# Optimization experiments

Measured on AMD Instinct MI355X. Metric: run time of the kernel, lower is better.

The kernel has to match this reference:

```python
import jax, jax.numpy as jnp
import numpy as np

B, L, E, MODES = 32, 2048, 512, 32  # batch, seq_len, d_model, kept Fourier modes (mode_select='low')


def setup_inputs() -> dict:
    key = jax.random.key(0)
    ks = jax.random.split(key, 6)
    scale = 1.0 / (E * E)  # FourierBlock scale = 1/(in_channels*out_channels), torch.rand init
    lin = E ** -0.5
    return {
        "queries": jax.random.normal(ks[0], (B, L, E), jnp.float32),
        "Wq": jax.random.normal(ks[1], (E, E), jnp.float32) * lin,
        "bq": jnp.zeros((E,), jnp.float32),
        "W1r": jax.random.uniform(ks[2], (E, E, MODES), jnp.float32) * scale,
        "W1i": jax.random.uniform(ks[3], (E, E, MODES), jnp.float32) * scale,
        "Wo": jax.random.normal(ks[4], (E, E), jnp.float32) * lin,
        "bo": jnp.zeros((E,), jnp.float32),
    }


def reference(queries, Wq, bq, W1r, W1i, Wo, bo):
    Bn, Ln, En = queries.shape
    # query projection
    q = queries @ Wq.T + bq                                    # (B, L, E)
    # FourierBlock: FFT along time, keep low `MODES` bins, complex channel mixing, inverse FFT
    xf = jnp.fft.rfft(q, axis=1)                               # (B, L//2+1, E) complex64
    W1 = (W1r + 1j * W1i).astype(jnp.complex64)                # (E_in, E_out, M)
    sel = xf[:, :MODES, :]                                     # (B, M, E) selected modes (mode_select='low')
    out_sel = jnp.einsum('bmi,iom->bmo', sel, W1)              # per-mode complex E x E mixing
    nfreq = Ln // 2 + 1
    out_ft = jnp.zeros((Bn, nfreq, En), jnp.complex64).at[:, :MODES, :].set(out_sel)
    x = jnp.fft.irfft(out_ft, n=Ln, axis=1)                    # (B, L, E) real
    # output projection (attn is None in the original; return the tensor output)
    return x @ Wo.T + bo
```

## Files before the change

### kernel.cpp

```cpp
#include <hip/hip_runtime.h>
#include <hip/hip_bf16.h>

typedef _Float16 f16;
typedef _Float16 f16x8 __attribute__((ext_vector_type(8)));
typedef _Float16 f16x4 __attribute__((ext_vector_type(4)));
typedef float f32x4 __attribute__((ext_vector_type(4)));

#define PADK 40
#define PADK2 72

#define W1SCALE 262144.0f
#define W1DESCALE 3.814697265625e-06f

static __device__ __forceinline__ f32x4 mfma16(f16x8 a, f16x8 b, f32x4 c) {
  return __builtin_amdgcn_mfma_f32_16x16x32_f16(a, b, c, 0, 0, 0);
}

__global__ __launch_bounds__(256) void k_tables(f16* __restrict__ FhT, f16* __restrict__ Gh) {
  int idx = blockIdx.x * 256 + threadIdx.x;
  const float w = 6.28318530717958647692f / 2048.0f;
  {
    int k2 = idx >> 11, l = idx & 2047;
    int k = k2 & 31;
    float th = (float)((k * l) & 2047) * w;
    float v = (k2 < 32) ? cosf(th) : -sinf(th);
    FhT[k2 * 2048 + l] = (f16)v;
  }
  {
    int l = idx >> 6, kk = idx & 63;
    int k = kk & 31;
    float th = (float)((k * l) & 2047) * w;
    float v;
    if (kk < 32) v = ((k == 0) ? 1.0f : 2.0f) * (1.0f / 2048.0f) * cosf(th);
    else         v = (k == 0) ? 0.0f : (-2.0f / 2048.0f) * sinf(th);
    Gh[l * 64 + kk] = (f16)v;
  }
}

__global__ __launch_bounds__(256) void k_cast_f16(const float* __restrict__ src,
                                                  f16* __restrict__ dst, int n4) {
  int i = blockIdx.x * 256 + threadIdx.x;
  if (i < n4) {
    float4 v = ((const float4*)src)[i];
    f16x4 o = {(f16)v.x, (f16)v.y, (f16)v.z, (f16)v.w};
    *(f16x4*)(dst + (size_t)i * 4) = o;
  }
}

__global__ __launch_bounds__(256) void k_dft_fwd(const f16* __restrict__ FhT,
                                                 const float* __restrict__ queries,
                                                 float* __restrict__ p32) {
  __shared__ __align__(16) f16 As[64 * PADK];
  __shared__ __align__(16) f16 Bs[64 * PADK];
  const int n0 = blockIdx.x * 64;
  const int b  = blockIdx.y;
  const int kb = blockIdx.z * 256;
  const int t = threadIdx.x;
  const int wid = t >> 6, lane = t & 63;
  const int mh = wid & 1, nh = wid >> 1;
  const int arow = t >> 2, ac8 = (t & 3) << 3;
  const int bcol = t & 63, bkg = t >> 6;
  f32x4 acc[2][2] = {};
  for (int k0 = kb; k0 < kb + 256; k0 += 32) {
    __syncthreads();
    *(f16x8*)(As + arow * PADK + ac8) =
        *(const f16x8*)(FhT + (size_t)arow * 2048 + k0 + ac8);
    const float* qp = queries + ((size_t)b * 2048 + k0 + bkg * 8) * 512 + n0 + bcol;
    float v[8];
#pragma unroll
    for (int r = 0; r < 8; ++r) v[r] = qp[(size_t)r * 512];
    f16x4 lo = {(f16)v[0], (f16)v[1], (f16)v[2], (f16)v[3]};
    f16x4 hi = {(f16)v[4], (f16)v[5], (f16)v[6], (f16)v[7]};
    *(f16x4*)(Bs + bcol * PADK + bkg * 8) = lo;
    *(f16x4*)(Bs + bcol * PADK + bkg * 8 + 4) = hi;
    __syncthreads();
    const int kofs = (lane >> 4) << 3;
    f16x8 a0 = *(const f16x8*)(As + (mh * 32 + 0  + (lane & 15)) * PADK + kofs);
    f16x8 a1 = *(const f16x8*)(As + (mh * 32 + 16 + (lane & 15)) * PADK + kofs);
    f16x8 b0 = *(const f16x8*)(Bs + (nh * 32 + 0  + (lane & 15)) * PADK + kofs);
    f16x8 b1 = *(const f16x8*)(Bs + (nh * 32 + 16 + (lane & 15)) * PADK + kofs);
    acc[0][0] = mfma16(a0, b0, acc[0][0]);
    acc[0][1] = mfma16(a0, b1, acc[0][1]);
    acc[1][0] = mfma16(a1, b0, acc[1][0]);
    acc[1][1] = mfma16(a1, b1, acc[1][1]);
  }
#pragma unroll
  for (int mf = 0; mf < 2; ++mf)
#pragma unroll
    for (int nf = 0; nf < 2; ++nf)
#pragma unroll
      for (int r = 0; r < 4; ++r) {
        int k2 = mh * 32 + mf * 16 + ((lane >> 4) << 2) + r;
        int col = n0 + nf * 16 + nh * 32 + (lane & 15);
        p32[((size_t)blockIdx.z * 2048 + b * 64 + k2) * 512 + col] = acc[mf][nf][r];
      }
}

__global__ __launch_bounds__(256) void k_reduceN(const float* __restrict__ p,
                                                 f16* __restrict__ dst, int ns) {
  size_t i4 = (size_t)blockIdx.x * 256 + threadIdx.x;
  float4 s = {0.f, 0.f, 0.f, 0.f};
  for (int c = 0; c < ns; ++c) {
    float4 v = ((const float4*)p)[(size_t)c * 262144 + i4];
    s.x += v.x; s.y += v.y; s.z += v.z; s.w += v.w;
  }
  f16x4 o = {(f16)s.x, (f16)s.y, (f16)s.z, (f16)s.w};
  *(f16x4*)(dst + i4 * 4) = o;
}

__global__ __launch_bounds__(256) void k_gemm_nk(const f16* __restrict__ A,
                                                 const f16* __restrict__ Bnk,
                                                 f16* __restrict__ C,
                                                 const float* __restrict__ bias0,
                                                 float bscale, int selt) {
  __shared__ __align__(16) f16 As[64 * PADK];
  __shared__ __align__(16) f16 Bs[32 * PADK];
  const int n0 = blockIdx.x * 32, m0 = blockIdx.y * 64;
  const int t = threadIdx.x;
  const int wid = t >> 6, lane = t & 63;
  const int mh = wid & 1, nh = wid >> 1;
  const int row = t >> 2, c8 = (t & 3) << 3;
  f32x4 acc[2] = {};
  for (int k0 = 0; k0 < 512; k0 += 32) {
    __syncthreads();
    *(f16x8*)(As + row * PADK + c8) =
        *(const f16x8*)(A + (size_t)(m0 + row) * 512 + k0 + c8);
    if (t < 128)
      *(f16x8*)(Bs + row * PADK + c8) =
          *(const f16x8*)(Bnk + (size_t)(n0 + row) * 512 + k0 + c8);
    __syncthreads();
    const int kofs = (lane >> 4) << 3;
    f16x8 a0 = *(const f16x8*)(As + (mh * 32 + 0  + (lane & 15)) * PADK + kofs);
    f16x8 a1 = *(const f16x8*)(As + (mh * 32 + 16 + (lane & 15)) * PADK + kofs);
    f16x8 b0 = *(const f16x8*)(Bs + (nh * 16 + (lane & 15)) * PADK + kofs);
    acc[0] = mfma16(a0, b0, acc[0]);
    acc[1] = mfma16(a1, b0, acc[1]);
  }
#pragma unroll
  for (int mf = 0; mf < 2; ++mf)
#pragma unroll
    for (int r = 0; r < 4; ++r) {
      int mg = m0 + mh * 32 + mf * 16 + ((lane >> 4) << 2) + r;
      int col = n0 + nh * 16 + (lane & 15);
      float cv = acc[mf][r];
      if (bias0 != nullptr && (mg & 63) == 0) cv += bscale * bias0[col];
      size_t didx = selt ? (((size_t)(mg & 63) * 32 + (mg >> 6)) * 512 + col)
                         : ((size_t)mg * 512 + col);
      C[didx] = (f16)cv;
    }
}

__global__ __launch_bounds__(512) void k_modes_fused(const float* __restrict__ W1r,
                                                     const float* __restrict__ W1i,
                                                     const f16* __restrict__ selT,
                                                     float* __restrict__ pmode) {
  __shared__ __align__(16) f16 Wst[2][16][648];
  const int o0 = blockIdx.x * 16, m0 = blockIdx.y * 16, is = blockIdx.z;
  const int t = threadIdx.x;
  const int lane = t & 63, wv = t >> 6;
  const int l15 = lane & 15, kq = lane >> 4, kofs = kq << 3;
  const int mq = t & 3, p = t >> 2;
  const int soo = p & 15, sib = p >> 4;
  f32x4 accR[2][2] = {}, accI[2][2] = {};
  const int ibase = is * 128;
  for (int ch = 0; ch < 4; ++ch) {
    const int i0c = ibase + ch * 32;
    __syncthreads();
#pragma unroll
    for (int ri = 0; ri < 2; ++ri) {
      const float* src = ri ? W1i : W1r;
#pragma unroll
      for (int qq = 0; qq < 4; ++qq) {
        int ii = sib + 8 * qq;
        const float4 v = *(const float4*)(src + (size_t)(i0c + ii) * 16384 +
                                          (o0 + soo) * 32 + m0 + mq * 4);
        f16* wp = &Wst[ri][mq * 4][soo * 40 + ii];
        wp[0 * 648] = (f16)(W1SCALE * v.x);
        wp[1 * 648] = (f16)(W1SCALE * v.y);
        wp[2 * 648] = (f16)(W1SCALE * v.z);
        wp[3 * 648] = (f16)(W1SCALE * v.w);
      }
    }
    __syncthreads();
#pragma unroll
    for (int ml = 0; ml < 2; ++ml) {
      const int mloc = 2 * wv + ml;
      const int mg = m0 + mloc;
      f16x8 ar0 = *(const f16x8*)(selT + ((size_t)mg * 32 + 0  + l15) * 512 + i0c + kofs);
      f16x8 ar1 = *(const f16x8*)(selT + ((size_t)mg * 32 + 16 + l15) * 512 + i0c + kofs);
      f16x8 ai0 = *(const f16x8*)(selT + ((size_t)(32 + mg) * 32 + 0  + l15) * 512 + i0c + kofs);
      f16x8 ai1 = *(const f16x8*)(selT + ((size_t)(32 + mg) * 32 + 16 + l15) * 512 + i0c + kofs);
      f16x8 br = *(const f16x8*)(&Wst[0][mloc][l15 * 40 + kofs]);
      f16x8 bi = *(const f16x8*)(&Wst[1][mloc][l15 * 40 + kofs]);
      f16x8 ain0 = -ai0, ain1 = -ai1;
      accR[ml][0] = mfma16(ar0,  br, accR[ml][0]);
      accR[ml][0] = mfma16(ain0, bi, accR[ml][0]);
      accI[ml][0] = mfma16(ar0,  bi, accI[ml][0]);
      accI[ml][0] = mfma16(ai0,  br, accI[ml][0]);
      accR[ml][1] = mfma16(ar1,  br, accR[ml][1]);
      accR[ml][1] = mfma16(ain1, bi, accR[ml][1]);
      accI[ml][1] = mfma16(ar1,  bi, accI[ml][1]);
      accI[ml][1] = mfma16(ai1,  br, accI[ml][1]);
    }
  }
#pragma unroll
  for (int ml = 0; ml < 2; ++ml) {
    const int mg = m0 + 2 * wv + ml;
#pragma unroll
    for (int bt = 0; bt < 2; ++bt)
#pragma unroll
      for (int r = 0; r < 4; ++r) {
        int bb = bt * 16 + kq * 4 + r;
        int og = o0 + l15;
        pmode[((size_t)is * 2048 + bb * 64 + mg) * 512 + og]      = accR[ml][bt][r];
        pmode[((size_t)is * 2048 + bb * 64 + 32 + mg) * 512 + og] = accI[ml][bt][r];
      }
  }
}

__global__ __launch_bounds__(256) void k_dft_inv(const f16* __restrict__ Gh,
                                                 const f16* __restrict__ u,
                                                 const float* __restrict__ bo,
                                                 float* __restrict__ out) {
  __shared__ __align__(16) f16 As[64 * PADK2];
  __shared__ __align__(16) f16 Bs[64 * PADK2];
  const int n0 = blockIdx.x * 64, l0 = blockIdx.y * 64, b = blockIdx.z;
  const int t = threadIdx.x, wid = t >> 6, lane = t & 63;
  const int mh = wid & 1, nh = wid >> 1;
#pragma unroll
  for (int p = 0; p < 2; ++p) {
    int v = t + 256 * p, row = v >> 3, c8 = (v & 7) << 3;
    *(f16x8*)(As + row * PADK2 + c8) = *(const f16x8*)(Gh + (size_t)(l0 + row) * 64 + c8);
  }
  {
    int col = t & 63, kg = t >> 6;
    const f16* up = u + ((size_t)b * 64 + kg * 16) * 512 + n0 + col;
    f16 vv[16];
#pragma unroll
    for (int s = 0; s < 16; ++s) vv[s] = up[(size_t)s * 512];
#pragma unroll
    for (int s4 = 0; s4 < 4; ++s4) {
      f16x4 pk = {vv[s4 * 4], vv[s4 * 4 + 1], vv[s4 * 4 + 2], vv[s4 * 4 + 3]};
      *(f16x4*)(Bs + col * PADK2 + kg * 16 + s4 * 4) = pk;
    }
  }
  __syncthreads();
  f32x4 acc[2][2] = {};
#pragma unroll
  for (int ks = 0; ks < 2; ++ks) {
    const int kofs = ks * 32 + ((lane >> 4) << 3);
    f16x8 a0 = *(const f16x8*)(As + (mh * 32 + 0  + (lane & 15)) * PADK2 + kofs);
    f16x8 a1 = *(const f16x8*)(As + (mh * 32 + 16 + (lane & 15)) * PADK2 + kofs);
    f16x8 b0 = *(const f16x8*)(Bs + (nh * 32 + 0  + (lane & 15)) * PADK2 + kofs);
    f16x8 b1 = *(const f16x8*)(Bs + (nh * 32 + 16 + (lane & 15)) * PADK2 + kofs);
    acc[0][0] = mfma16(a0, b0, acc[0][0]);
    acc[0][1] = mfma16(a0, b1, acc[0][1]);
    acc[1][0] = mfma16(a1, b0, acc[1][0]);
    acc[1][1] = mfma16(a1, b1, acc[1][1]);
  }
#pragma unroll
  for (int mf = 0; mf < 2; ++mf)
#pragma unroll
    for (int nf = 0; nf < 2; ++nf)
#pragma unroll
      for (int r = 0; r < 4; ++r) {
        int l = l0 + mh * 32 + mf * 16 + ((lane >> 4) << 2) + r;
        int col = n0 + nh * 32 + nf * 16 + (lane & 15);
        float cv = acc[mf][nf][r] * W1DESCALE + bo[col];
        out[((size_t)b * 2048 + l) * 512 + col] = cv;
      }
}

extern "C" void kernel_launch(void* const* d_in, const int* in_sizes, int n_in,
                              void* d_out, int out_size, void* d_ws, size_t ws_size,
                              hipStream_t stream) {
  const float* queries = (const float*)d_in[0];
  const float* Wq      = (const float*)d_in[1];
  const float* bq      = (const float*)d_in[2];
  const float* W1r     = (const float*)d_in[3];
  const float* W1i     = (const float*)d_in[4];
  const float* Wo      = (const float*)d_in[5];
  const float* bo      = (const float*)d_in[6];
  float* out           = (float*)d_out;

  char* ws = (char*)d_ws;
  size_t off = 0;
  auto alloc = [&](size_t bytes) {
    off = (off + 255) & ~(size_t)255;
    char* p = ws + off;
    off += bytes;
    return p;
  };
  f16* FhT    = (f16*)alloc((size_t)64 * 2048 * 2);
  f16* Gh     = (f16*)alloc((size_t)2048 * 64 * 2);
  f16* Wq16   = (f16*)alloc((size_t)512 * 512 * 2);
  f16* Wo16   = (f16*)alloc((size_t)512 * 512 * 2);
  float* p32  = (float*)alloc((size_t)8 * 2048 * 512 * 4);
  f16* t16    = (f16*)alloc((size_t)2048 * 512 * 2);
  f16* selT   = (f16*)alloc((size_t)2048 * 512 * 2);
  float* pmode= (float*)alloc((size_t)4 * 2048 * 512 * 4);
  f16* osel   = (f16*)alloc((size_t)2048 * 512 * 2);
  f16* u16    = (f16*)alloc((size_t)2048 * 512 * 2);

  hipLaunchKernelGGL(k_tables, dim3(512), dim3(256), 0, stream, FhT, Gh);
  hipLaunchKernelGGL(k_cast_f16, dim3(256), dim3(256), 0, stream, Wq, Wq16, 65536);
  hipLaunchKernelGGL(k_cast_f16, dim3(256), dim3(256), 0, stream, Wo, Wo16, 65536);
  hipLaunchKernelGGL(k_dft_fwd, dim3(8, 32, 8), dim3(256), 0, stream, FhT, queries, p32);
  hipLaunchKernelGGL(k_reduceN, dim3(1024), dim3(256), 0, stream, p32, t16, 8);
  hipLaunchKernelGGL(k_gemm_nk, dim3(16, 32), dim3(256), 0, stream, t16, Wq16, selT,
                     bq, 2048.0f, 1);
  hipLaunchKernelGGL(k_modes_fused, dim3(32, 2, 4), dim3(512), 0, stream,
                     W1r, W1i, selT, pmode);
  hipLaunchKernelGGL(k_reduceN, dim3(1024), dim3(256), 0, stream, pmode, osel, 4);
  hipLaunchKernelGGL(k_gemm_nk, dim3(16, 32), dim3(256), 0, stream, osel, Wo16, u16,
                     (const float*)nullptr, 0.0f, 0);
  hipLaunchKernelGGL(k_dft_inv, dim3(8, 32, 32), dim3(256), 0, stream, Gh, u16, bo, out);
}
```

Before: 143.5 us.

## Deepen K tiles to 128 in DFT and GEMM kernels, merge prep kernels

The forward DFT and the NK GEMM now stage 128-wide K chunks in shared memory per sync instead of 32, doing four MFMA k-steps between barriers. The forward DFT split-K factor drops from 8 to 4, which halves the partial-sum buffer and the reduction work. The table-building and weight-cast kernels are merged into one launch. In exchange, each block uses more shared memory and registers (32 floats per thread for the queries load), which can lower occupancy, and the forward DFT grid is half as large.

```diff
diff --git a/kernel.cpp b/kernel.cpp
--- a/kernel.cpp
+++ b/kernel.cpp
@@ -6,7 +6,7 @@
 typedef _Float16 f16x4 __attribute__((ext_vector_type(4)));
 typedef float f32x4 __attribute__((ext_vector_type(4)));
 
-#define PADK 40
+#define QPAD 136
 #define PADK2 72
 
 #define W1SCALE 262144.0f
@@ -16,7 +16,11 @@
   return __builtin_amdgcn_mfma_f32_16x16x32_f16(a, b, c, 0, 0, 0);
 }
 
-__global__ __launch_bounds__(256) void k_tables(f16* __restrict__ FhT, f16* __restrict__ Gh) {
+__global__ __launch_bounds__(256) void k_prep(f16* __restrict__ FhT, f16* __restrict__ Gh,
+                                              const float* __restrict__ Wq,
+                                              const float* __restrict__ Wo,
+                                              f16* __restrict__ Wq16,
+                                              f16* __restrict__ Wo16) {
   int idx = blockIdx.x * 256 + threadIdx.x;
   const float w = 6.28318530717958647692f / 2048.0f;
   {
@@ -35,12 +39,10 @@
     else         v = (k == 0) ? 0.0f : (-2.0f / 2048.0f) * sinf(th);
     Gh[l * 64 + kk] = (f16)v;
   }
-}
-
-__global__ __launch_bounds__(256) void k_cast_f16(const float* __restrict__ src,
-                                                  f16* __restrict__ dst, int n4) {
-  int i = blockIdx.x * 256 + threadIdx.x;
-  if (i < n4) {
+  {
+    const float* src = (idx < 65536) ? Wq : Wo;
+    f16* dst = (idx < 65536) ? Wq16 : Wo16;
+    int i = idx & 65535;
     float4 v = ((const float4*)src)[i];
     f16x4 o = {(f16)v.x, (f16)v.y, (f16)v.z, (f16)v.w};
     *(f16x4*)(dst + (size_t)i * 4) = o;
@@ -50,39 +52,48 @@
 __global__ __launch_bounds__(256) void k_dft_fwd(const f16* __restrict__ FhT,
                                                  const float* __restrict__ queries,
                                                  float* __restrict__ p32) {
-  __shared__ __align__(16) f16 As[64 * PADK];
-  __shared__ __align__(16) f16 Bs[64 * PADK];
+  __shared__ __align__(16) f16 As[64 * QPAD];
+  __shared__ __align__(16) f16 Bs[64 * QPAD];
   const int n0 = blockIdx.x * 64;
   const int b  = blockIdx.y;
-  const int kb = blockIdx.z * 256;
+  const int kb = blockIdx.z * 512;
   const int t = threadIdx.x;
   const int wid = t >> 6, lane = t & 63;
   const int mh = wid & 1, nh = wid >> 1;
-  const int arow = t >> 2, ac8 = (t & 3) << 3;
+  const int l15 = lane & 15, kq = lane >> 4;
+  const int arow = t >> 2, ac0 = (t & 3) << 5;
   const int bcol = t & 63, bkg = t >> 6;
   f32x4 acc[2][2] = {};
-  for (int k0 = kb; k0 < kb + 256; k0 += 32) {
-    __syncthreads();
-    *(f16x8*)(As + arow * PADK + ac8) =
-        *(const f16x8*)(FhT + (size_t)arow * 2048 + k0 + ac8);
-    const float* qp = queries + ((size_t)b * 2048 + k0 + bkg * 8) * 512 + n0 + bcol;
-    float v[8];
-#pragma unroll
-    for (int r = 0; r < 8; ++r) v[r] = qp[(size_t)r * 512];
-    f16x4 lo = {(f16)v[0], (f16)v[1], (f16)v[2], (f16)v[3]};
-    f16x4 hi = {(f16)v[4], (f16)v[5], (f16)v[6], (f16)v[7]};
-    *(f16x4*)(Bs + bcol * PADK + bkg * 8) = lo;
-    *(f16x4*)(Bs + bcol * PADK + bkg * 8 + 4) = hi;
-    __syncthreads();
-    const int kofs = (lane >> 4) << 3;
-    f16x8 a0 = *(const f16x8*)(As + (mh * 32 + 0  + (lane & 15)) * PADK + kofs);
-    f16x8 a1 = *(const f16x8*)(As + (mh * 32 + 16 + (lane & 15)) * PADK + kofs);
-    f16x8 b0 = *(const f16x8*)(Bs + (nh * 32 + 0  + (lane & 15)) * PADK + kofs);
-    f16x8 b1 = *(const f16x8*)(Bs + (nh * 32 + 16 + (lane & 15)) * PADK + kofs);
-    acc[0][0] = mfma16(a0, b0, acc[0][0]);
-    acc[0][1] = mfma16(a0, b1, acc[0][1]);
-    acc[1][0] = mfma16(a1, b0, acc[1][0]);
-    acc[1][1] = mfma16(a1, b1, acc[1][1]);
+  for (int ph = 0; ph < 4; ++ph) {
+    const int k0 = kb + ph * 128;
+    __syncthreads();
+#pragma unroll
+    for (int j = 0; j < 4; ++j)
+      *(f16x8*)(As + arow * QPAD + ac0 + j * 8) =
+          *(const f16x8*)(FhT + (size_t)arow * 2048 + k0 + ac0 + j * 8);
+    const float* qp = queries + ((size_t)b * 2048 + k0 + bkg * 32) * 512 + n0 + bcol;
+    float v[32];
+#pragma unroll
+    for (int r = 0; r < 32; ++r) v[r] = qp[(size_t)r * 512];
+#pragma unroll
+    for (int s = 0; s < 4; ++s) {
+      f16x8 pk = {(f16)v[s*8+0], (f16)v[s*8+1], (f16)v[s*8+2], (f16)v[s*8+3],
+                  (f16)v[s*8+4], (f16)v[s*8+5], (f16)v[s*8+6], (f16)v[s*8+7]};
+      *(f16x8*)(Bs + bcol * QPAD + bkg * 32 + s * 8) = pk;
+    }
+    __syncthreads();
+#pragma unroll
+    for (int ks = 0; ks < 4; ++ks) {
+      const int kofs = ks * 32 + kq * 8;
+      f16x8 a0 = *(const f16x8*)(As + (mh * 32 + 0  + l15) * QPAD + kofs);
+      f16x8 a1 = *(const f16x8*)(As + (mh * 32 + 16 + l15) * QPAD + kofs);
+      f16x8 b0 = *(const f16x8*)(Bs + (nh * 32 + 0  + l15) * QPAD + kofs);
+      f16x8 b1 = *(const f16x8*)(Bs + (nh * 32 + 16 + l15) * QPAD + kofs);
+      acc[0][0] = mfma16(a0, b0, acc[0][0]);
+      acc[0][1] = mfma16(a0, b1, acc[0][1]);
+      acc[1][0] = mfma16(a1, b0, acc[1][0]);
+      acc[1][1] = mfma16(a1, b1, acc[1][1]);
+    }
   }
 #pragma unroll
   for (int mf = 0; mf < 2; ++mf)
@@ -90,8 +101,8 @@
     for (int nf = 0; nf < 2; ++nf)
 #pragma unroll
       for (int r = 0; r < 4; ++r) {
-        int k2 = mh * 32 + mf * 16 + ((lane >> 4) << 2) + r;
-        int col = n0 + nf * 16 + nh * 32 + (lane & 15);
+        int k2 = mh * 32 + mf * 16 + kq * 4 + r;
+        int col = n0 + nh * 32 + nf * 16 + l15;
         p32[((size_t)blockIdx.z * 2048 + b * 64 + k2) * 512 + col] = acc[mf][nf][r];
       }
 }
@@ -113,35 +124,46 @@
                                                  f16* __restrict__ C,
                                                  const float* __restrict__ bias0,
                                                  float bscale, int selt) {
-  __shared__ __align__(16) f16 As[64 * PADK];
-  __shared__ __align__(16) f16 Bs[32 * PADK];
+  __shared__ __align__(16) f16 As[64 * QPAD];
+  __shared__ __align__(16) f16 Bs[32 * QPAD];
   const int n0 = blockIdx.x * 32, m0 = blockIdx.y * 64;
   const int t = threadIdx.x;
   const int wid = t >> 6, lane = t & 63;
   const int mh = wid & 1, nh = wid >> 1;
-  const int row = t >> 2, c8 = (t & 3) << 3;
+  const int l15 = lane & 15, kq = lane >> 4;
+  const int row = t >> 2, c0 = (t & 3) << 5;
   f32x4 acc[2] = {};
-  for (int k0 = 0; k0 < 512; k0 += 32) {
-    __syncthreads();
-    *(f16x8*)(As + row * PADK + c8) =
-        *(const f16x8*)(A + (size_t)(m0 + row) * 512 + k0 + c8);
-    if (t < 128)
-      *(f16x8*)(Bs + row * PADK + c8) =
-          *(const f16x8*)(Bnk + (size_t)(n0 + row) * 512 + k0 + c8);
-    __syncthreads();
-    const int kofs = (lane >> 4) << 3;
-    f16x8 a0 = *(const f16x8*)(As + (mh * 32 + 0  + (lane & 15)) * PADK + kofs);
-    f16x8 a1 = *(const f16x8*)(As + (mh * 32 + 16 + (lane & 15)) * PADK + kofs);
-    f16x8 b0 = *(const f16x8*)(Bs + (nh * 16 + (lane & 15)) * PADK + kofs);
-    acc[0] = mfma16(a0, b0, acc[0]);
-    acc[1] = mfma16(a1, b0, acc[1]);
+  for (int ph = 0; ph < 4; ++ph) {
+    const int k0 = ph * 128;
+    __syncthreads();
+#pragma unroll
+    for (int j = 0; j < 4; ++j)
+      *(f16x8*)(As + row * QPAD + c0 + j * 8) =
+          *(const f16x8*)(A + (size_t)(m0 + row) * 512 + k0 + c0 + j * 8);
+    if (t < 128) {
+      const int br = t >> 2, bc0 = (t & 3) << 5;
+#pragma unroll
+      for (int j = 0; j < 4; ++j)
+        *(f16x8*)(Bs + br * QPAD + bc0 + j * 8) =
+            *(const f16x8*)(Bnk + (size_t)(n0 + br) * 512 + k0 + bc0 + j * 8);
+    }
+    __syncthreads();
+#pragma unroll
+    for (int ks = 0; ks < 4; ++ks) {
+      const int kofs = ks * 32 + kq * 8;
+      f16x8 a0 = *(const f16x8*)(As + (mh * 32 + 0  + l15) * QPAD + kofs);
+      f16x8 a1 = *(const f16x8*)(As + (mh * 32 + 16 + l15) * QPAD + kofs);
+      f16x8 b0 = *(const f16x8*)(Bs + (nh * 16 + l15) * QPAD + kofs);
+      acc[0] = mfma16(a0, b0, acc[0]);
+      acc[1] = mfma16(a1, b0, acc[1]);
+    }
   }
 #pragma unroll
   for (int mf = 0; mf < 2; ++mf)
 #pragma unroll
     for (int r = 0; r < 4; ++r) {
-      int mg = m0 + mh * 32 + mf * 16 + ((lane >> 4) << 2) + r;
-      int col = n0 + nh * 16 + (lane & 15);
+      int mg = m0 + mh * 32 + mf * 16 + kq * 4 + r;
+      int col = n0 + nh * 16 + l15;
       float cv = acc[mf][r];
       if (bias0 != nullptr && (mg & 63) == 0) cv += bscale * bias0[col];
       size_t didx = selt ? (((size_t)(mg & 63) * 32 + (mg >> 6)) * 512 + col)
@@ -295,18 +317,16 @@
   f16* Gh     = (f16*)alloc((size_t)2048 * 64 * 2);
   f16* Wq16   = (f16*)alloc((size_t)512 * 512 * 2);
   f16* Wo16   = (f16*)alloc((size_t)512 * 512 * 2);
-  float* p32  = (float*)alloc((size_t)8 * 2048 * 512 * 4);
+  float* p32  = (float*)alloc((size_t)4 * 2048 * 512 * 4);
   f16* t16    = (f16*)alloc((size_t)2048 * 512 * 2);
   f16* selT   = (f16*)alloc((size_t)2048 * 512 * 2);
   float* pmode= (float*)alloc((size_t)4 * 2048 * 512 * 4);
   f16* osel   = (f16*)alloc((size_t)2048 * 512 * 2);
   f16* u16    = (f16*)alloc((size_t)2048 * 512 * 2);
 
-  hipLaunchKernelGGL(k_tables, dim3(512), dim3(256), 0, stream, FhT, Gh);
-  hipLaunchKernelGGL(k_cast_f16, dim3(256), dim3(256), 0, stream, Wq, Wq16, 65536);
-  hipLaunchKernelGGL(k_cast_f16, dim3(256), dim3(256), 0, stream, Wo, Wo16, 65536);
-  hipLaunchKernelGGL(k_dft_fwd, dim3(8, 32, 8), dim3(256), 0, stream, FhT, queries, p32);
-  hipLaunchKernelGGL(k_reduceN, dim3(1024), dim3(256), 0, stream, p32, t16, 8);
+  hipLaunchKernelGGL(k_prep, dim3(512), dim3(256), 0, stream, FhT, Gh, Wq, Wo, Wq16, Wo16);
+  hipLaunchKernelGGL(k_dft_fwd, dim3(8, 32, 4), dim3(256), 0, stream, FhT, queries, p32);
+  hipLaunchKernelGGL(k_reduceN, dim3(1024), dim3(256), 0, stream, p32, t16, 4);
   hipLaunchKernelGGL(k_gemm_nk, dim3(16, 32), dim3(256), 0, stream, t16, Wq16, selT,
                      bq, 2048.0f, 1);
   hipLaunchKernelGGL(k_modes_fused, dim3(32, 2, 4), dim3(512), 0, stream,
```

Measured after the change: 126.5 us. 1.13x faster.
